# Kernel tuning notes

Hardware: AMD Instinct MI355X
Metric: run time of the kernel (lower is better)

The kernel has to match this reference:

```python
import jax, jax.numpy as jnp
import numpy as np

B, IN_DIM, HID = 4096, 1024, 1024


def _linear(x, W, b):
    # torch nn.Linear: y = x @ W.T + b, W is [out, in]
    return x @ W.T + b


def setup_inputs() -> dict:
    key = jax.random.key(0)
    ks = jax.random.split(key, 15)
    s_in = 1.0 / np.sqrt(IN_DIM + HID)
    s_x = 1.0 / np.sqrt(IN_DIM)
    s_h = 1.0 / np.sqrt(HID)
    return {
        "x": jax.random.normal(ks[0], (B, IN_DIM), jnp.float32),
        "h_prev": jax.random.normal(ks[1], (B, HID), jnp.float32),
        "c_prev": jax.random.normal(ks[2], (B, HID), jnp.float32),
        "Wi": jax.random.normal(ks[3], (HID, IN_DIM + HID), jnp.float32) * s_in,
        "bi": jax.random.normal(ks[4], (HID,), jnp.float32) * s_in,
        "Wf": jax.random.normal(ks[5], (HID, IN_DIM + HID), jnp.float32) * s_in,
        "bf": jax.random.normal(ks[6], (HID,), jnp.float32) * s_in,
        "Wo": jax.random.normal(ks[7], (HID, IN_DIM + HID), jnp.float32) * s_in,
        "bo": jax.random.normal(ks[8], (HID,), jnp.float32) * s_in,
        "Wxs": jax.random.normal(ks[9], (HID, IN_DIM), jnp.float32) * s_x,
        "bxs": jax.random.normal(ks[10], (HID,), jnp.float32) * s_x,
        "Wxg": jax.random.normal(ks[11], (HID, IN_DIM), jnp.float32) * s_x,
        "bxg": jax.random.normal(ks[12], (HID,), jnp.float32) * s_x,
        "Whg": jax.random.normal(ks[13], (HID, HID), jnp.float32) * s_h,
        "bhg": jax.random.normal(ks[14], (HID,), jnp.float32) * s_h,
    }


def reference(x, h_prev, c_prev, Wi, bi, Wf, bf, Wo, bo, Wxs, bxs, Wxg, bxg, Whg, bhg):
    # Fuse the three (in_dim+hid)->hid gate GEMMs into one concatenated GEMM.
    concat = jnp.concatenate([x, h_prev], axis=-1)          # [B, in_dim+hid]
    W_ifo = jnp.concatenate([Wi, Wf, Wo], axis=0)           # [3*hid, in_dim+hid]
    b_ifo = jnp.concatenate([bi, bf, bo], axis=0)           # [3*hid]
    gates = jax.nn.sigmoid(_linear(concat, W_ifo, b_ifo))   # [B, 3*hid]
    i_t, f_t, o_t = jnp.split(gates, 3, axis=-1)
    s_t = _linear(x, Wxs, bxs)
    cand_lin = _linear(x, Wxg, bxg) + _linear(h_prev, Whg, bhg)
    g_t = jnp.tanh(s_t * cand_lin)
    # refined=False branch
    c_t = f_t * c_prev + i_t * g_t
    h_t = o_t * jnp.tanh(c_t)
    return (h_t, c_t)
```

## Files before the change

kernel.cpp:

```cpp
#include <hip/hip_runtime.h>

typedef unsigned short u16;
typedef __attribute__((ext_vector_type(8))) __bf16 bf16x8;
typedef __attribute__((ext_vector_type(4))) float f32x4;
typedef __attribute__((ext_vector_type(4))) unsigned short u16x4;

#define AS1 __attribute__((address_space(1)))
#define AS3 __attribute__((address_space(3)))

#define OB_X    0L
#define OB_H    4194304L
#define OB_WI   8388608L
#define OB_WF   10485760L
#define OB_WO   12582912L
#define OB_WXS  14680064L
#define OB_WXG  15728640L
#define OB_WHG  16777216L
#define BLOB_EL 17825792L

__device__ __forceinline__ u16 f2b(float f) {
    unsigned u = __float_as_uint(f);
    u += 0x7fffu + ((u >> 16) & 1u);
    return (u16)(u >> 16);
}

__global__ __launch_bounds__(256) void convert_all(
    const float* __restrict__ x, const float* __restrict__ h,
    const float* __restrict__ Wi, const float* __restrict__ Wf,
    const float* __restrict__ Wo, const float* __restrict__ Wxs,
    const float* __restrict__ Wxg, const float* __restrict__ Whg,
    u16* __restrict__ blob)
{
    long e = ((long)blockIdx.x * 256 + threadIdx.x) * 8;
    const float* src; long off;
    if      (e < OB_H)   { src = x;   off = e; }
    else if (e < OB_WI)  { src = h;   off = e - OB_H; }
    else if (e < OB_WF)  { src = Wi;  off = e - OB_WI; }
    else if (e < OB_WO)  { src = Wf;  off = e - OB_WF; }
    else if (e < OB_WXS) { src = Wo;  off = e - OB_WO; }
    else if (e < OB_WXG) { src = Wxs; off = e - OB_WXS; }
    else if (e < OB_WHG) { src = Wxg; off = e - OB_WXG; }
    else                 { src = Whg; off = e - OB_WHG; }
    f32x4 v0 = *(const f32x4*)(src + off);
    f32x4 v1 = *(const f32x4*)(src + off + 4);
    u16x4 o0, o1;
    o0.x = f2b(v0.x); o0.y = f2b(v0.y); o0.z = f2b(v0.z); o0.w = f2b(v0.w);
    o1.x = f2b(v1.x); o1.y = f2b(v1.y); o1.z = f2b(v1.z); o1.w = f2b(v1.w);
    *(u16x4*)(blob + e) = o0;
    *(u16x4*)(blob + e + 4) = o1;
}

__device__ __forceinline__ void stageB(u16* dst, const u16* src, int ld,
                                       int t, int er, int gsw) {
#pragma unroll
    for (int it = 0; it < 2; ++it) {
        const int row = it * 32 + er;
        __builtin_amdgcn_global_load_lds(
            (AS1 void*)(src + row * ld + gsw),
            (AS3 void*)(dst + (it * 256 + t) * 8), 16, 0, 0);
    }
}

__device__ __forceinline__ float sigf(float z) {
    return 1.f / (1.f + __expf(-z));
}

__global__ __launch_bounds__(256, 2) void srulstm_fused(
    const u16* __restrict__ blob,
    const float* __restrict__ c_prev,
    const float* __restrict__ bi, const float* __restrict__ bfv,
    const float* __restrict__ bo, const float* __restrict__ bxs,
    const float* __restrict__ bxg, const float* __restrict__ bhg,
    float* __restrict__ out)
{
    __shared__ __align__(16) u16 As[128 * 64];
    __shared__ __align__(16) u16 Bs[5 * 64 * 64];

    const u16* x   = blob + OB_X;
    const u16* h   = blob + OB_H;

    const int t = threadIdx.x;
    const int j0 = blockIdx.x * 64;
    const int m0 = blockIdx.y * 128;

    const u16* w0   = blob + OB_WI  + j0 * 2048;
    const u16* w1   = blob + OB_WF  + j0 * 2048;
    const u16* w2   = blob + OB_WO  + j0 * 2048;
    const u16* w3lo = blob + OB_WXG + j0 * 1024;
    const u16* w3hi = blob + OB_WHG + j0 * 1024;
    const u16* w4   = blob + OB_WXS + j0 * 1024;

    const u16* aLo = x + m0 * 1024;
    const u16* aHi = h + m0 * 1024;

    const int lane = t & 63;
    const int wave = t >> 6;
    const int wm = (wave >> 1) << 6;
    const int wn = (wave & 1) << 5;
    const int fr = lane & 15;
    const int fq = lane >> 4;
    const int r7 = fr & 7;

    f32x4 acc[5][4][2] = {};

    const int er = t >> 3;
    const int gsw = (((t & 7) ^ (er & 7)) << 3);

    for (int k0 = 0; k0 < 2048; k0 += 64) {
        const u16* aSrc = ((k0 < 1024) ? aLo : aHi) + (k0 & 1023);
#pragma unroll
        for (int it = 0; it < 4; ++it) {
            const int row = it * 32 + er;
            __builtin_amdgcn_global_load_lds(
                (AS1 void*)(aSrc + row * 1024 + gsw),
                (AS3 void*)(As + (it * 256 + t) * 8), 16, 0, 0);
        }
        stageB(Bs,         w0 + k0, 2048, t, er, gsw);
        stageB(Bs + 4096,  w1 + k0, 2048, t, er, gsw);
        stageB(Bs + 8192,  w2 + k0, 2048, t, er, gsw);
        stageB(Bs + 12288, (k0 < 1024) ? (w3lo + k0) : (w3hi + (k0 - 1024)),
               1024, t, er, gsw);
        if (k0 < 1024)
            stageB(Bs + 16384, w4 + k0, 1024, t, er, gsw);
        __syncthreads();
#pragma unroll
        for (int kk = 0; kk < 64; kk += 32) {
            const int sw = ((((kk >> 3) + fq) ^ r7) << 3);
            bf16x8 a[4];
#pragma unroll
            for (int mi = 0; mi < 4; ++mi)
                a[mi] = *(const bf16x8*)(As + (wm + mi * 16 + fr) * 64 + sw);
#pragma unroll
            for (int s = 0; s < 4; ++s) {
                bf16x8 b0 = *(const bf16x8*)(Bs + s * 4096 + (wn + fr) * 64 + sw);
                bf16x8 b1 = *(const bf16x8*)(Bs + s * 4096 + (wn + 16 + fr) * 64 + sw);
#pragma unroll
                for (int mi = 0; mi < 4; ++mi) {
                    acc[s][mi][0] = __builtin_amdgcn_mfma_f32_16x16x32_bf16(
                        a[mi], b0, acc[s][mi][0], 0, 0, 0);
                    acc[s][mi][1] = __builtin_amdgcn_mfma_f32_16x16x32_bf16(
                        a[mi], b1, acc[s][mi][1], 0, 0, 0);
                }
            }
            if (k0 < 1024) {
                bf16x8 b0 = *(const bf16x8*)(Bs + 16384 + (wn + fr) * 64 + sw);
                bf16x8 b1 = *(const bf16x8*)(Bs + 16384 + (wn + 16 + fr) * 64 + sw);
#pragma unroll
                for (int mi = 0; mi < 4; ++mi) {
                    acc[4][mi][0] = __builtin_amdgcn_mfma_f32_16x16x32_bf16(
                        a[mi], b0, acc[4][mi][0], 0, 0, 0);
                    acc[4][mi][1] = __builtin_amdgcn_mfma_f32_16x16x32_bf16(
                        a[mi], b1, acc[4][mi][1], 0, 0, 0);
                }
            }
        }
        __syncthreads();
    }

    const int orow = m0 + wm + (fq << 2);
    const int ocol = j0 + wn + fr;
#pragma unroll
    for (int ni = 0; ni < 2; ++ni) {
        const int col = ocol + ni * 16;
        const float bi_v = bi[col],  bf_v = bfv[col], bo_v = bo[col];
        const float bs_v = bxs[col], bg_v = bxg[col], bh_v = bhg[col];
#pragma unroll
        for (int mi = 0; mi < 4; ++mi) {
#pragma unroll
            for (int r = 0; r < 4; ++r) {
                const long idx = (long)(orow + mi * 16 + r) * 1024 + col;
                const float cp = c_prev[idx];
                const float i_t = sigf(acc[0][mi][ni][r] + bi_v);
                const float f_t = sigf(acc[1][mi][ni][r] + bf_v);
                const float o_t = sigf(acc[2][mi][ni][r] + bo_v);
                const float cand = acc[3][mi][ni][r] + bg_v + bh_v;
                const float s_t  = acc[4][mi][ni][r] + bs_v;
                const float g_t = tanhf(s_t * cand);
                const float c_t = f_t * cp + i_t * g_t;
                const float h_t = o_t * tanhf(c_t);
                out[idx] = h_t;
                out[4194304L + idx] = c_t;
            }
        }
    }
}

extern "C" void kernel_launch(void* const* d_in, const int* in_sizes, int n_in,
                              void* d_out, int out_size, void* d_ws, size_t ws_size,
                              hipStream_t stream)
{
    u16* blob = (u16*)d_ws;
    float* out = (float*)d_out;

    const long convBlocks = BLOB_EL / 8 / 256;

    convert_all<<<dim3(convBlocks), dim3(256), 0, stream>>>(
        (const float*)d_in[0], (const float*)d_in[1], (const float*)d_in[3],
        (const float*)d_in[5], (const float*)d_in[7], (const float*)d_in[9],
        (const float*)d_in[11], (const float*)d_in[13], blob);

    srulstm_fused<<<dim3(16, 32), dim3(256), 0, stream>>>(
        blob, (const float*)d_in[2], (const float*)d_in[4], (const float*)d_in[6],
        (const float*)d_in[8], (const float*)d_in[10], (const float*)d_in[12],
        (const float*)d_in[14], out);
}
```

Before: 226.6 us.

## Double-buffer LDS tiles with 512-thread blocks and 256-row M tiles

Splits the fused gate GEMM into stage and compute helpers. It double-buffers the A and B LDS tiles so the asynchronous global-to-LDS loads for the next K slice are issued while MFMAs run on the current one. The block grows to 512 threads covering 256 rows, which halves the grid and lets twice as many rows share each weight tile. LDS use rises to about 144KB, so only one block fits per CU. The launch-bounds hint of two 512-thread blocks may cap registers below what the 160-float accumulator needs, risking spills. The bf16 conversion kernel now writes one 16-byte vector store instead of two 8-byte stores.

```diff
diff --git a/kernel.cpp b/kernel.cpp
--- a/kernel.cpp
+++ b/kernel.cpp
@@ -4,6 +4,7 @@
 typedef __attribute__((ext_vector_type(8))) __bf16 bf16x8;
 typedef __attribute__((ext_vector_type(4))) float f32x4;
 typedef __attribute__((ext_vector_type(4))) unsigned short u16x4;
+typedef __attribute__((ext_vector_type(8))) unsigned short u16x8;
 
 #define AS1 __attribute__((address_space(1)))
 #define AS3 __attribute__((address_space(3)))
@@ -43,29 +44,83 @@
     else                 { src = Whg; off = e - OB_WHG; }
     f32x4 v0 = *(const f32x4*)(src + off);
     f32x4 v1 = *(const f32x4*)(src + off + 4);
-    u16x4 o0, o1;
-    o0.x = f2b(v0.x); o0.y = f2b(v0.y); o0.z = f2b(v0.z); o0.w = f2b(v0.w);
-    o1.x = f2b(v1.x); o1.y = f2b(v1.y); o1.z = f2b(v1.z); o1.w = f2b(v1.w);
-    *(u16x4*)(blob + e) = o0;
-    *(u16x4*)(blob + e + 4) = o1;
-}
-
-__device__ __forceinline__ void stageB(u16* dst, const u16* src, int ld,
-                                       int t, int er, int gsw) {
-#pragma unroll
-    for (int it = 0; it < 2; ++it) {
-        const int row = it * 32 + er;
-        __builtin_amdgcn_global_load_lds(
-            (AS1 void*)(src + row * ld + gsw),
-            (AS3 void*)(dst + (it * 256 + t) * 8), 16, 0, 0);
-    }
+    u16x8 o;
+    o[0] = f2b(v0.x); o[1] = f2b(v0.y); o[2] = f2b(v0.z); o[3] = f2b(v0.w);
+    o[4] = f2b(v1.x); o[5] = f2b(v1.y); o[6] = f2b(v1.z); o[7] = f2b(v1.w);
+    *(u16x8*)(blob + e) = o;
 }
 
 __device__ __forceinline__ float sigf(float z) {
     return 1.f / (1.f + __expf(-z));
 }
 
-__global__ __launch_bounds__(256, 2) void srulstm_fused(
+__device__ __forceinline__ void stage_tile(
+    u16* As, u16* Bs, int k0,
+    const u16* aLo, const u16* aHi,
+    const u16* w0, const u16* w1, const u16* w2,
+    const u16* w3lo, const u16* w3hi, const u16* w4,
+    int t, int er, int gsw)
+{
+    const u16* aSrc = ((k0 < 1024) ? aLo : aHi) + (k0 & 1023) + gsw;
+#pragma unroll
+    for (int it = 0; it < 4; ++it) {
+        __builtin_amdgcn_global_load_lds(
+            (AS1 void*)(aSrc + (it * 64 + er) * 1024),
+            (AS3 void*)(As + (it * 512 + t) * 8), 16, 0, 0);
+    }
+    __builtin_amdgcn_global_load_lds((AS1 void*)(w0 + k0 + er * 2048 + gsw),
+        (AS3 void*)(Bs + t * 8), 16, 0, 0);
+    __builtin_amdgcn_global_load_lds((AS1 void*)(w1 + k0 + er * 2048 + gsw),
+        (AS3 void*)(Bs + 4096 + t * 8), 16, 0, 0);
+    __builtin_amdgcn_global_load_lds((AS1 void*)(w2 + k0 + er * 2048 + gsw),
+        (AS3 void*)(Bs + 8192 + t * 8), 16, 0, 0);
+    const u16* w3 = (k0 < 1024) ? (w3lo + k0) : (w3hi + (k0 - 1024));
+    __builtin_amdgcn_global_load_lds((AS1 void*)(w3 + er * 1024 + gsw),
+        (AS3 void*)(Bs + 12288 + t * 8), 16, 0, 0);
+    if (k0 < 1024)
+        __builtin_amdgcn_global_load_lds((AS1 void*)(w4 + k0 + er * 1024 + gsw),
+            (AS3 void*)(Bs + 16384 + t * 8), 16, 0, 0);
+}
+
+__device__ __forceinline__ void compute_tile(
+    const u16* As, const u16* Bs, bool seg4,
+    int wm, int wn, int fr, int fq, int r7,
+    f32x4 (&acc)[5][4][2])
+{
+#pragma unroll
+    for (int kk = 0; kk < 64; kk += 32) {
+        const int sw = ((((kk >> 3) + fq) ^ r7) << 3);
+        bf16x8 a[4];
+#pragma unroll
+        for (int mi = 0; mi < 4; ++mi)
+            a[mi] = *(const bf16x8*)(As + (wm + mi * 16 + fr) * 64 + sw);
+#pragma unroll
+        for (int s = 0; s < 4; ++s) {
+            bf16x8 b0 = *(const bf16x8*)(Bs + s * 4096 + (wn + fr) * 64 + sw);
+            bf16x8 b1 = *(const bf16x8*)(Bs + s * 4096 + (wn + 16 + fr) * 64 + sw);
+#pragma unroll
+            for (int mi = 0; mi < 4; ++mi) {
+                acc[s][mi][0] = __builtin_amdgcn_mfma_f32_16x16x32_bf16(
+                    a[mi], b0, acc[s][mi][0], 0, 0, 0);
+                acc[s][mi][1] = __builtin_amdgcn_mfma_f32_16x16x32_bf16(
+                    a[mi], b1, acc[s][mi][1], 0, 0, 0);
+            }
+        }
+        if (seg4) {
+            bf16x8 b0 = *(const bf16x8*)(Bs + 16384 + (wn + fr) * 64 + sw);
+            bf16x8 b1 = *(const bf16x8*)(Bs + 16384 + (wn + 16 + fr) * 64 + sw);
+#pragma unroll
+            for (int mi = 0; mi < 4; ++mi) {
+                acc[4][mi][0] = __builtin_amdgcn_mfma_f32_16x16x32_bf16(
+                    a[mi], b0, acc[4][mi][0], 0, 0, 0);
+                acc[4][mi][1] = __builtin_amdgcn_mfma_f32_16x16x32_bf16(
+                    a[mi], b1, acc[4][mi][1], 0, 0, 0);
+            }
+        }
+    }
+}
+
+__global__ __launch_bounds__(512, 2) void srulstm_fused(
     const u16* __restrict__ blob,
     const float* __restrict__ c_prev,
     const float* __restrict__ bi, const float* __restrict__ bfv,
@@ -73,15 +128,15 @@
     const float* __restrict__ bxg, const float* __restrict__ bhg,
     float* __restrict__ out)
 {
-    __shared__ __align__(16) u16 As[128 * 64];
-    __shared__ __align__(16) u16 Bs[5 * 64 * 64];
-
-    const u16* x   = blob + OB_X;
-    const u16* h   = blob + OB_H;
+    __shared__ __align__(16) u16 As[2][256 * 64];
+    __shared__ __align__(16) u16 Bs[2][5 * 64 * 64];
+
+    const u16* x = blob + OB_X;
+    const u16* h = blob + OB_H;
 
     const int t = threadIdx.x;
     const int j0 = blockIdx.x * 64;
-    const int m0 = blockIdx.y * 128;
+    const int m0 = blockIdx.y * 256;
 
     const u16* w0   = blob + OB_WI  + j0 * 2048;
     const u16* w1   = blob + OB_WF  + j0 * 2048;
@@ -101,59 +156,23 @@
     const int fq = lane >> 4;
     const int r7 = fr & 7;
 
-    f32x4 acc[5][4][2] = {};
-
     const int er = t >> 3;
     const int gsw = (((t & 7) ^ (er & 7)) << 3);
 
-    for (int k0 = 0; k0 < 2048; k0 += 64) {
-        const u16* aSrc = ((k0 < 1024) ? aLo : aHi) + (k0 & 1023);
-#pragma unroll
-        for (int it = 0; it < 4; ++it) {
-            const int row = it * 32 + er;
-            __builtin_amdgcn_global_load_lds(
-                (AS1 void*)(aSrc + row * 1024 + gsw),
-                (AS3 void*)(As + (it * 256 + t) * 8), 16, 0, 0);
-        }
-        stageB(Bs,         w0 + k0, 2048, t, er, gsw);
-        stageB(Bs + 4096,  w1 + k0, 2048, t, er, gsw);
-        stageB(Bs + 8192,  w2 + k0, 2048, t, er, gsw);
-        stageB(Bs + 12288, (k0 < 1024) ? (w3lo + k0) : (w3hi + (k0 - 1024)),
-               1024, t, er, gsw);
-        if (k0 < 1024)
-            stageB(Bs + 16384, w4 + k0, 1024, t, er, gsw);
+    f32x4 acc[5][4][2] = {};
+
+    stage_tile(As[0], Bs[0], 0, aLo, aHi, w0, w1, w2, w3lo, w3hi, w4, t, er, gsw);
+    __syncthreads();
+
+    for (int k0 = 0; k0 < 2048; k0 += 128) {
+        stage_tile(As[1], Bs[1], k0 + 64,
+                   aLo, aHi, w0, w1, w2, w3lo, w3hi, w4, t, er, gsw);
+        compute_tile(As[0], Bs[0], k0 < 1024, wm, wn, fr, fq, r7, acc);
         __syncthreads();
-#pragma unroll
-        for (int kk = 0; kk < 64; kk += 32) {
-            const int sw = ((((kk >> 3) + fq) ^ r7) << 3);
-            bf16x8 a[4];
-#pragma unroll
-            for (int mi = 0; mi < 4; ++mi)
-                a[mi] = *(const bf16x8*)(As + (wm + mi * 16 + fr) * 64 + sw);
-#pragma unroll
-            for (int s = 0; s < 4; ++s) {
-                bf16x8 b0 = *(const bf16x8*)(Bs + s * 4096 + (wn + fr) * 64 + sw);
-                bf16x8 b1 = *(const bf16x8*)(Bs + s * 4096 + (wn + 16 + fr) * 64 + sw);
-#pragma unroll
-                for (int mi = 0; mi < 4; ++mi) {
-                    acc[s][mi][0] = __builtin_amdgcn_mfma_f32_16x16x32_bf16(
-                        a[mi], b0, acc[s][mi][0], 0, 0, 0);
-                    acc[s][mi][1] = __builtin_amdgcn_mfma_f32_16x16x32_bf16(
-                        a[mi], b1, acc[s][mi][1], 0, 0, 0);
-                }
-            }
-            if (k0 < 1024) {
-                bf16x8 b0 = *(const bf16x8*)(Bs + 16384 + (wn + fr) * 64 + sw);
-                bf16x8 b1 = *(const bf16x8*)(Bs + 16384 + (wn + 16 + fr) * 64 + sw);
-#pragma unroll
-                for (int mi = 0; mi < 4; ++mi) {
-                    acc[4][mi][0] = __builtin_amdgcn_mfma_f32_16x16x32_bf16(
-                        a[mi], b0, acc[4][mi][0], 0, 0, 0);
-                    acc[4][mi][1] = __builtin_amdgcn_mfma_f32_16x16x32_bf16(
-                        a[mi], b1, acc[4][mi][1], 0, 0, 0);
-                }
-            }
-        }
+        if (k0 + 128 < 2048)
+            stage_tile(As[0], Bs[0], k0 + 128,
+                       aLo, aHi, w0, w1, w2, w3lo, w3hi, w4, t, er, gsw);
+        compute_tile(As[1], Bs[1], (k0 + 64) < 1024, wm, wn, fr, fq, r7, acc);
         __syncthreads();
     }
 
@@ -199,7 +218,7 @@
         (const float*)d_in[5], (const float*)d_in[7], (const float*)d_in[9],
         (const float*)d_in[11], (const float*)d_in[13], blob);
 
-    srulstm_fused<<<dim3(16, 32), dim3(256), 0, stream>>>(
+    srulstm_fused<<<dim3(16, 16), dim3(512), 0, stream>>>(
         blob, (const float*)d_in[2], (const float*)d_in[4], (const float*)d_in[6],
         (const float*)d_in[8], (const float*)d_in[10], (const float*)d_in[12],
         (const float*)d_in[14], out);
```

Measured after the change: 247.3 us. 1.09x slower.

## Double-buffer LDS tiles with async prefetch and enlarge block to 256 rows

Applied to the files above, without the earlier changes.

The fused gate GEMM now uses 512-thread blocks covering 256 batch rows, with two LDS buffers for the A and B tiles. The next K-slice is prefetched via global_load_lds while the current one is computed. Hand-written vmcnt waits and s_barrier replace __syncthreads, so compute no longer stalls on every global load. This raises LDS use to about 144KB, limiting each CU to one block, and always stages the Wxs tile even in the second half of K, where those loads are wasted.

```diff
diff --git a/kernel.cpp b/kernel.cpp
--- a/kernel.cpp
+++ b/kernel.cpp
@@ -50,22 +50,11 @@
     *(u16x4*)(blob + e + 4) = o1;
 }
 
-__device__ __forceinline__ void stageB(u16* dst, const u16* src, int ld,
-                                       int t, int er, int gsw) {
-#pragma unroll
-    for (int it = 0; it < 2; ++it) {
-        const int row = it * 32 + er;
-        __builtin_amdgcn_global_load_lds(
-            (AS1 void*)(src + row * ld + gsw),
-            (AS3 void*)(dst + (it * 256 + t) * 8), 16, 0, 0);
-    }
-}
-
 __device__ __forceinline__ float sigf(float z) {
     return 1.f / (1.f + __expf(-z));
 }
 
-__global__ __launch_bounds__(256, 2) void srulstm_fused(
+__global__ __launch_bounds__(512) void srulstm_fused(
     const u16* __restrict__ blob,
     const float* __restrict__ c_prev,
     const float* __restrict__ bi, const float* __restrict__ bfv,
@@ -73,15 +62,15 @@
     const float* __restrict__ bxg, const float* __restrict__ bhg,
     float* __restrict__ out)
 {
-    __shared__ __align__(16) u16 As[128 * 64];
-    __shared__ __align__(16) u16 Bs[5 * 64 * 64];
-
-    const u16* x   = blob + OB_X;
-    const u16* h   = blob + OB_H;
+    __shared__ __align__(16) u16 As[2][256 * 64];
+    __shared__ __align__(16) u16 Bs[2][5 * 64 * 64];
+
+    const u16* x = blob + OB_X;
+    const u16* h = blob + OB_H;
 
     const int t = threadIdx.x;
     const int j0 = blockIdx.x * 64;
-    const int m0 = blockIdx.y * 128;
+    const int m0 = blockIdx.y * 256;
 
     const u16* w0   = blob + OB_WI  + j0 * 2048;
     const u16* w1   = blob + OB_WF  + j0 * 2048;
@@ -101,39 +90,44 @@
     const int fq = lane >> 4;
     const int r7 = fr & 7;
 
-    f32x4 acc[5][4][2] = {};
-
     const int er = t >> 3;
     const int gsw = (((t & 7) ^ (er & 7)) << 3);
 
-    for (int k0 = 0; k0 < 2048; k0 += 64) {
-        const u16* aSrc = ((k0 < 1024) ? aLo : aHi) + (k0 & 1023);
-#pragma unroll
-        for (int it = 0; it < 4; ++it) {
-            const int row = it * 32 + er;
+    f32x4 acc[5][4][2] = {};
+
+    auto stage = [&](u16* An, u16* Bn, int kS) {
+        const int kSc = (kS < 2048) ? kS : 1984;
+        const u16* aSrc = ((kSc < 1024) ? aLo : aHi) + (kSc & 1023);
+#pragma unroll
+        for (int it = 0; it < 4; ++it)
             __builtin_amdgcn_global_load_lds(
-                (AS1 void*)(aSrc + row * 1024 + gsw),
-                (AS3 void*)(As + (it * 256 + t) * 8), 16, 0, 0);
-        }
-        stageB(Bs,         w0 + k0, 2048, t, er, gsw);
-        stageB(Bs + 4096,  w1 + k0, 2048, t, er, gsw);
-        stageB(Bs + 8192,  w2 + k0, 2048, t, er, gsw);
-        stageB(Bs + 12288, (k0 < 1024) ? (w3lo + k0) : (w3hi + (k0 - 1024)),
-               1024, t, er, gsw);
-        if (k0 < 1024)
-            stageB(Bs + 16384, w4 + k0, 1024, t, er, gsw);
-        __syncthreads();
+                (AS1 void*)(aSrc + (it * 64 + er) * 1024 + gsw),
+                (AS3 void*)(An + (it * 512 + t) * 8), 16, 0, 0);
+        __builtin_amdgcn_global_load_lds((AS1 void*)(w0 + kSc + er * 2048 + gsw),
+            (AS3 void*)(Bn + t * 8), 16, 0, 0);
+        __builtin_amdgcn_global_load_lds((AS1 void*)(w1 + kSc + er * 2048 + gsw),
+            (AS3 void*)(Bn + 4096 + t * 8), 16, 0, 0);
+        __builtin_amdgcn_global_load_lds((AS1 void*)(w2 + kSc + er * 2048 + gsw),
+            (AS3 void*)(Bn + 8192 + t * 8), 16, 0, 0);
+        const u16* w3 = (kSc < 1024) ? (w3lo + kSc) : (w3hi + (kSc - 1024));
+        __builtin_amdgcn_global_load_lds((AS1 void*)(w3 + er * 1024 + gsw),
+            (AS3 void*)(Bn + 12288 + t * 8), 16, 0, 0);
+        __builtin_amdgcn_global_load_lds((AS1 void*)(w4 + (kSc & 1023) + er * 1024 + gsw),
+            (AS3 void*)(Bn + 16384 + t * 8), 16, 0, 0);
+    };
+
+    auto compute = [&](const u16* Ac, const u16* Bc, bool seg4) {
 #pragma unroll
         for (int kk = 0; kk < 64; kk += 32) {
             const int sw = ((((kk >> 3) + fq) ^ r7) << 3);
             bf16x8 a[4];
 #pragma unroll
             for (int mi = 0; mi < 4; ++mi)
-                a[mi] = *(const bf16x8*)(As + (wm + mi * 16 + fr) * 64 + sw);
+                a[mi] = *(const bf16x8*)(Ac + (wm + mi * 16 + fr) * 64 + sw);
 #pragma unroll
             for (int s = 0; s < 4; ++s) {
-                bf16x8 b0 = *(const bf16x8*)(Bs + s * 4096 + (wn + fr) * 64 + sw);
-                bf16x8 b1 = *(const bf16x8*)(Bs + s * 4096 + (wn + 16 + fr) * 64 + sw);
+                bf16x8 b0 = *(const bf16x8*)(Bc + s * 4096 + (wn + fr) * 64 + sw);
+                bf16x8 b1 = *(const bf16x8*)(Bc + s * 4096 + (wn + 16 + fr) * 64 + sw);
 #pragma unroll
                 for (int mi = 0; mi < 4; ++mi) {
                     acc[s][mi][0] = __builtin_amdgcn_mfma_f32_16x16x32_bf16(
@@ -142,9 +136,9 @@
                         a[mi], b1, acc[s][mi][1], 0, 0, 0);
                 }
             }
-            if (k0 < 1024) {
-                bf16x8 b0 = *(const bf16x8*)(Bs + 16384 + (wn + fr) * 64 + sw);
-                bf16x8 b1 = *(const bf16x8*)(Bs + 16384 + (wn + 16 + fr) * 64 + sw);
+            if (seg4) {
+                bf16x8 b0 = *(const bf16x8*)(Bc + 16384 + (wn + fr) * 64 + sw);
+                bf16x8 b1 = *(const bf16x8*)(Bc + 16384 + (wn + 16 + fr) * 64 + sw);
 #pragma unroll
                 for (int mi = 0; mi < 4; ++mi) {
                     acc[4][mi][0] = __builtin_amdgcn_mfma_f32_16x16x32_bf16(
@@ -154,8 +148,21 @@
                 }
             }
         }
-        __syncthreads();
+    };
+
+    stage(As[0], Bs[0], 0);
+
+    for (int k0 = 0; k0 < 2048; k0 += 128) {
+        stage(As[1], Bs[1], k0 + 64);
+        asm volatile("s_waitcnt vmcnt(9)\n\ts_barrier" ::: "memory");
+        compute(As[0], Bs[0], k0 < 1024);
+        asm volatile("s_barrier" ::: "memory");
+        stage(As[0], Bs[0], k0 + 128);
+        asm volatile("s_waitcnt vmcnt(9)\n\ts_barrier" ::: "memory");
+        compute(As[1], Bs[1], (k0 + 64) < 1024);
+        asm volatile("s_barrier" ::: "memory");
     }
+    asm volatile("s_waitcnt vmcnt(0)" ::: "memory");
 
     const int orow = m0 + wm + (fq << 2);
     const int ocol = j0 + wn + fr;
@@ -199,7 +206,7 @@
         (const float*)d_in[5], (const float*)d_in[7], (const float*)d_in[9],
         (const float*)d_in[11], (const float*)d_in[13], blob);
 
-    srulstm_fused<<<dim3(16, 32), dim3(256), 0, stream>>>(
+    srulstm_fused<<<dim3(16, 16), dim3(512), 0, stream>>>(
         blob, (const float*)d_in[2], (const float*)d_in[4], (const float*)d_in[6],
         (const float*)d_in[8], (const float*)d_in[10], (const float*)d_in[12],
         (const float*)d_in[14], out);
```

After: 255.3 us. +12.7%, slower.
